# Kernel tuning notes

Hardware: AMD Instinct MI355X
Metric: run time of the kernel (lower is better)

The kernel has to match this reference:

```python
import jax, jax.numpy as jnp
import numpy as np

N, SD, HD, CD, AD = 8192, 64, 128, 32, 8  # num_agents, state_dim, hidden_dim, comm_dim, action_dim
NOISE_SCALE = 0.01


def _l2norm(x, axis):
    # F.normalize: x / max(||x||_2, eps), eps=1e-12
    return x / jnp.maximum(jnp.linalg.norm(x, axis=axis, keepdims=True), 1e-12)


def setup_inputs() -> dict:
    key = jax.random.key(0)
    ks = jax.random.split(key, 12)
    def w(k, shape, scale=0.05):
        return jax.random.normal(k, shape, jnp.float32) * scale
    return {
        "states": jax.random.normal(ks[0], (N, SD), jnp.float32),
        "noise": jax.random.normal(ks[1], (N, HD), jnp.float32),
        # ReasoningCore: Linear(SD+CD->HD), ReLU, Linear(HD->HD)
        "W1": w(ks[2], (SD + CD, HD)), "b1": jnp.zeros((HD,), jnp.float32),
        "W2": w(ks[3], (HD, HD)),      "b2": jnp.zeros((HD,), jnp.float32),
        # CommunicationModule encoder: Linear(HD->CD)
        "Wc": w(ks[4], (HD, CD)), "bc": jnp.zeros((CD,), jnp.float32),
        # GNNLayer: Linear(HD->HD)
        "Wg": w(ks[5], (HD, HD)), "bg": jnp.zeros((HD,), jnp.float32),
        # Policy: Linear(HD->AD)
        "Wp": w(ks[6], (HD, AD)), "bp": jnp.zeros((AD,), jnp.float32),
        # Value: Linear(HD->1)
        "Wv": w(ks[7], (HD, 1)), "bv": jnp.zeros((1,), jnp.float32),
        # RoleHead: Linear(HD->3)
        "Wr": w(ks[8], (HD, 3)), "br": jnp.zeros((3,), jnp.float32),
    }


def reference(states, noise, W1, b1, W2, b2, Wc, bc, Wg, bg, Wp, bp, Wv, bv, Wr, br):
    def core(x, comm):
        h = jax.nn.relu(jnp.concatenate([x, comm], axis=-1) @ W1 + b1)  # [N, HD]
        return h @ W2 + b2

    comm0 = jnp.zeros((N, CD), states.dtype)
    H = core(states, comm0)                                   # [N, HD]
    msgs = _l2norm(H @ Wc + bc, axis=1)                       # [N, CD]
    comm = jnp.broadcast_to(msgs.mean(axis=0, keepdims=True), (N, CD))
    H = core(states, comm)                                    # [N, HD]
    adj = jnp.ones((N, N), states.dtype) / N                  # dense uniform adjacency
    H = jax.nn.relu((adj @ H) @ Wg + bg)                      # GNN layer
    H = _l2norm(H + noise * NOISE_SCALE, axis=1)
    actions = jnp.tanh(H @ Wp + bp)                           # [N, AD]
    values = H @ Wv + bv                                      # [N, 1]
    role_probs = jax.nn.softmax(H @ Wr + br, axis=-1)         # [N, 3]
    return (H, actions, values, role_probs)
```

## Files before the change

kernel.cpp:

```cpp
#include <hip/hip_runtime.h>
#include <math.h>

#define N_AG 8192
#define SD 64
#define HD 128
#define CD 32
#define AD 8

#define P_OFF     0
#define W2C_OFF   (N_AG*HD)
#define BCP_OFF   (W2C_OFF + HD*CD)
#define MSUM_OFF  (BCP_OFF + CD)
#define HSUM_OFF  (MSUM_OFF + CD)
#define G_OFF     (HSUM_OFF + HD)

__global__ void k0_pre(const float* __restrict__ W2, const float* __restrict__ b2,
                       const float* __restrict__ Wc, const float* __restrict__ bc,
                       float* __restrict__ ws) {
    float* W2c  = ws + W2C_OFF;
    float* bcp  = ws + BCP_OFF;
    float* msum = ws + MSUM_OFF;
    float* hsum = ws + HSUM_OFF;
    int tid = threadIdx.x;
    if (blockIdx.x < 16) {
        int idx = blockIdx.x * 256 + tid;
        int i = idx >> 5, c = idx & 31;
        float s = 0.f;
        #pragma unroll 8
        for (int k = 0; k < HD; ++k) s += W2[i*HD + k] * Wc[k*CD + c];
        W2c[idx] = s;
    } else {
        if (tid < CD) {
            float s = bc[tid];
            for (int k = 0; k < HD; ++k) s += b2[k] * Wc[k*CD + tid];
            bcp[tid] = s;
            msum[tid] = 0.f;
        }
        if (tid >= 64 && tid < 64 + HD) hsum[tid - 64] = 0.f;
    }
}

#define APB1 16
__global__ void k1_phaseA(const float* __restrict__ X, const float* __restrict__ W1,
                          const float* __restrict__ b1, float* __restrict__ ws) {
    const float* W2c = ws + W2C_OFF;
    const float* bcp = ws + BCP_OFF;
    float* P    = ws + P_OFF;
    float* msum = ws + MSUM_OFF;
    __shared__ float sX[APB1][SD];
    __shared__ float sH[APB1][HD + 1];
    __shared__ float sM[APB1][CD + 1];
    __shared__ float sR[APB1];
    int tid = threadIdx.x;
    int a0 = blockIdx.x * APB1;
    for (int i = tid; i < APB1 * SD; i += 256) sX[i >> 6][i & 63] = X[a0 * SD + i];
    __syncthreads();
    for (int idx = tid; idx < APB1 * HD; idx += 256) {
        int ag = idx >> 7, c = idx & 127;
        float s = b1[c];
        #pragma unroll
        for (int k = 0; k < SD; ++k) s += sX[ag][k] * W1[k*HD + c];
        P[(a0 + ag)*HD + c] = s;
        sH[ag][c] = fmaxf(s, 0.f);
    }
    __syncthreads();
    for (int idx = tid; idx < APB1 * CD; idx += 256) {
        int ag = idx >> 5, c = idx & 31;
        float s = bcp[c];
        #pragma unroll 16
        for (int k = 0; k < HD; ++k) s += sH[ag][k] * W2c[k*CD + c];
        sM[ag][c] = s;
    }
    __syncthreads();
    if (tid < APB1) {
        float ss = 0.f;
        for (int c = 0; c < CD; ++c) { float m = sM[tid][c]; ss += m * m; }
        sR[tid] = 1.f / fmaxf(sqrtf(ss), 1e-12f);
    }
    __syncthreads();
    if (tid < CD) {
        float s = 0.f;
        for (int ag = 0; ag < APB1; ++ag) s += sM[ag][tid] * sR[ag];
        atomicAdd(&msum[tid], s);
    }
}

#define APB2 16
__global__ void k2_phaseB(const float* __restrict__ W1, float* __restrict__ ws) {
    const float* P    = ws + P_OFF;
    const float* msum = ws + MSUM_OFF;
    float* hsum = ws + HSUM_OFF;
    __shared__ float cvec[HD];
    __shared__ float red[256];
    int tid = threadIdx.x;
    if (tid < HD) {
        float s = 0.f;
        #pragma unroll
        for (int k = 0; k < CD; ++k) s += msum[k] * W1[(SD + k)*HD + tid];
        cvec[tid] = s * (1.f / (float)N_AG);
    }
    __syncthreads();
    int c = tid & 127, half = tid >> 7;
    int a0 = blockIdx.x * APB2;
    float part = 0.f;
    for (int ag = half; ag < APB2; ag += 2)
        part += fmaxf(P[(a0 + ag)*HD + c] + cvec[c], 0.f);
    red[tid] = part;
    __syncthreads();
    if (tid < HD) atomicAdd(&hsum[tid], red[tid] + red[tid + 128]);
}

__global__ void k3_gvec(const float* __restrict__ W2, const float* __restrict__ b2,
                        const float* __restrict__ Wg, const float* __restrict__ bg,
                        float* __restrict__ ws) {
    const float* hsum = ws + HSUM_OFF;
    float* g = ws + G_OFF;
    __shared__ float hm[HD];
    __shared__ float u[HD];
    int t = threadIdx.x;
    hm[t] = hsum[t] * (1.f / (float)N_AG);
    __syncthreads();
    float s = b2[t];
    #pragma unroll 16
    for (int k = 0; k < HD; ++k) s += hm[k] * W2[k*HD + t];
    u[t] = s;
    __syncthreads();
    float s2 = bg[t];
    #pragma unroll 16
    for (int k = 0; k < HD; ++k) s2 += u[k] * Wg[k*HD + t];
    g[t] = fmaxf(s2, 0.f);
}

__global__ void k4_out(const float* __restrict__ noise,
                       const float* __restrict__ Wp, const float* __restrict__ bp,
                       const float* __restrict__ Wv, const float* __restrict__ bv,
                       const float* __restrict__ Wr, const float* __restrict__ br,
                       const float* __restrict__ ws, float* __restrict__ out) {
    const float* g = ws + G_OFF;
    int gtid = blockIdx.x * blockDim.x + threadIdx.x;
    int a = gtid >> 6;
    int lane = threadIdx.x & 63;
    if (a >= N_AG) return;
    float v0 = g[lane]      + 0.01f * noise[a*HD + lane];
    float v1 = g[lane + 64] + 0.01f * noise[a*HD + 64 + lane];
    float ss = v0 * v0 + v1 * v1;
    #pragma unroll
    for (int off = 32; off; off >>= 1) ss += __shfl_xor(ss, off);
    float rinv = 1.f / fmaxf(sqrtf(ss), 1e-12f);
    float h0 = v0 * rinv, h1 = v1 * rinv;
    float* outH = out;
    float* outA = out + N_AG * HD;
    float* outV = outA + N_AG * AD;
    float* outR = outV + N_AG;
    outH[a*HD + lane]      = h0;
    outH[a*HD + 64 + lane] = h1;
    float acc[12];
    #pragma unroll
    for (int j = 0; j < 8; ++j)
        acc[j] = h0 * Wp[lane*AD + j] + h1 * Wp[(lane + 64)*AD + j];
    acc[8] = h0 * Wv[lane] + h1 * Wv[lane + 64];
    #pragma unroll
    for (int j = 0; j < 3; ++j)
        acc[9 + j] = h0 * Wr[lane*3 + j] + h1 * Wr[(lane + 64)*3 + j];
    #pragma unroll
    for (int j = 0; j < 12; ++j) {
        #pragma unroll
        for (int off = 32; off; off >>= 1) acc[j] += __shfl_xor(acc[j], off);
    }
    if (lane < 8) {
        outA[a*AD + lane] = tanhf(acc[lane] + bp[lane]);
    } else if (lane == 8) {
        outV[a] = acc[8] + bv[0];
    } else if (lane >= 9 && lane < 12) {
        float l0 = acc[9] + br[0], l1 = acc[10] + br[1], l2 = acc[11] + br[2];
        float m = fmaxf(l0, fmaxf(l1, l2));
        float e0 = expf(l0 - m), e1 = expf(l1 - m), e2 = expf(l2 - m);
        float denom = e0 + e1 + e2;
        float mine = (lane == 9) ? e0 : (lane == 10) ? e1 : e2;
        outR[a*3 + (lane - 9)] = mine / denom;
    }
}

extern "C" void kernel_launch(void* const* d_in, const int* in_sizes, int n_in,
                              void* d_out, int out_size, void* d_ws, size_t ws_size,
                              hipStream_t stream) {
    const float* states = (const float*)d_in[0];
    const float* noise  = (const float*)d_in[1];
    const float* W1 = (const float*)d_in[2];
    const float* b1 = (const float*)d_in[3];
    const float* W2 = (const float*)d_in[4];
    const float* b2 = (const float*)d_in[5];
    const float* Wc = (const float*)d_in[6];
    const float* bc = (const float*)d_in[7];
    const float* Wg = (const float*)d_in[8];
    const float* bg = (const float*)d_in[9];
    const float* Wp = (const float*)d_in[10];
    const float* bp = (const float*)d_in[11];
    const float* Wv = (const float*)d_in[12];
    const float* bv = (const float*)d_in[13];
    const float* Wr = (const float*)d_in[14];
    const float* br = (const float*)d_in[15];
    float* ws  = (float*)d_ws;
    float* out = (float*)d_out;

    hipLaunchKernelGGL(k0_pre,   dim3(17),           dim3(256), 0, stream, W2, b2, Wc, bc, ws);
    hipLaunchKernelGGL(k1_phaseA,dim3(N_AG / APB1),  dim3(256), 0, stream, states, W1, b1, ws);
    hipLaunchKernelGGL(k2_phaseB,dim3(N_AG / APB2),  dim3(256), 0, stream, W1, ws);
    hipLaunchKernelGGL(k3_gvec,  dim3(1),            dim3(128), 0, stream, W2, b2, Wg, bg, ws);
    hipLaunchKernelGGL(k4_out,   dim3(N_AG / 4),     dim3(256), 0, stream, noise, Wp, bp, Wv, bv, Wr, br, ws, out);
}
```

Before: 142.1 us.

## Vectorize phase kernels, fuse gvec into output kernel, transpose head weights

Rewrites the pipeline. k3 (the single-block g-vector kernel) is folded into the output kernel, and every block recomputes the 128-wide g vector redundantly. The per-agent kernels now use float4 register tiling with two agents per thread. The policy, value and role weights are pre-transposed into a packed workspace array so the heads become per-lane dot products instead of 12 full-wavefront shuffle reductions. This removes one launch and many shuffles, but each of the 512 output blocks now repeats two 128x128 matvecs.

```diff
diff --git a/kernel.cpp b/kernel.cpp
--- a/kernel.cpp
+++ b/kernel.cpp
@@ -8,176 +8,231 @@
 #define AD 8
 
 #define P_OFF     0
-#define W2C_OFF   (N_AG*HD)
-#define BCP_OFF   (W2C_OFF + HD*CD)
+#define W2CT_OFF  (N_AG*HD)
+#define WALLT_OFF (W2CT_OFF + CD*HD)
+#define BALL_OFF  (WALLT_OFF + 12*HD)
+#define BCP_OFF   (BALL_OFF + 16)
 #define MSUM_OFF  (BCP_OFF + CD)
 #define HSUM_OFF  (MSUM_OFF + CD)
-#define G_OFF     (HSUM_OFF + HD)
 
 __global__ void k0_pre(const float* __restrict__ W2, const float* __restrict__ b2,
                        const float* __restrict__ Wc, const float* __restrict__ bc,
-                       float* __restrict__ ws) {
-    float* W2c  = ws + W2C_OFF;
-    float* bcp  = ws + BCP_OFF;
-    float* msum = ws + MSUM_OFF;
-    float* hsum = ws + HSUM_OFF;
-    int tid = threadIdx.x;
-    if (blockIdx.x < 16) {
-        int idx = blockIdx.x * 256 + tid;
-        int i = idx >> 5, c = idx & 31;
-        float s = 0.f;
-        #pragma unroll 8
-        for (int k = 0; k < HD; ++k) s += W2[i*HD + k] * Wc[k*CD + c];
-        W2c[idx] = s;
-    } else {
-        if (tid < CD) {
-            float s = bc[tid];
-            for (int k = 0; k < HD; ++k) s += b2[k] * Wc[k*CD + tid];
-            bcp[tid] = s;
-            msum[tid] = 0.f;
-        }
-        if (tid >= 64 && tid < 64 + HD) hsum[tid - 64] = 0.f;
-    }
-}
-
-#define APB1 16
-__global__ void k1_phaseA(const float* __restrict__ X, const float* __restrict__ W1,
-                          const float* __restrict__ b1, float* __restrict__ ws) {
-    const float* W2c = ws + W2C_OFF;
-    const float* bcp = ws + BCP_OFF;
-    float* P    = ws + P_OFF;
-    float* msum = ws + MSUM_OFF;
-    __shared__ float sX[APB1][SD];
-    __shared__ float sH[APB1][HD + 1];
-    __shared__ float sM[APB1][CD + 1];
-    __shared__ float sR[APB1];
-    int tid = threadIdx.x;
-    int a0 = blockIdx.x * APB1;
-    for (int i = tid; i < APB1 * SD; i += 256) sX[i >> 6][i & 63] = X[a0 * SD + i];
-    __syncthreads();
-    for (int idx = tid; idx < APB1 * HD; idx += 256) {
-        int ag = idx >> 7, c = idx & 127;
-        float s = b1[c];
-        #pragma unroll
-        for (int k = 0; k < SD; ++k) s += sX[ag][k] * W1[k*HD + c];
-        P[(a0 + ag)*HD + c] = s;
-        sH[ag][c] = fmaxf(s, 0.f);
-    }
-    __syncthreads();
-    for (int idx = tid; idx < APB1 * CD; idx += 256) {
-        int ag = idx >> 5, c = idx & 31;
-        float s = bcp[c];
-        #pragma unroll 16
-        for (int k = 0; k < HD; ++k) s += sH[ag][k] * W2c[k*CD + c];
-        sM[ag][c] = s;
-    }
-    __syncthreads();
-    if (tid < APB1) {
-        float ss = 0.f;
-        for (int c = 0; c < CD; ++c) { float m = sM[tid][c]; ss += m * m; }
-        sR[tid] = 1.f / fmaxf(sqrtf(ss), 1e-12f);
-    }
-    __syncthreads();
-    if (tid < CD) {
-        float s = 0.f;
-        for (int ag = 0; ag < APB1; ++ag) s += sM[ag][tid] * sR[ag];
-        atomicAdd(&msum[tid], s);
-    }
-}
-
-#define APB2 16
-__global__ void k2_phaseB(const float* __restrict__ W1, float* __restrict__ ws) {
-    const float* P    = ws + P_OFF;
-    const float* msum = ws + MSUM_OFF;
-    float* hsum = ws + HSUM_OFF;
-    __shared__ float cvec[HD];
-    __shared__ float red[256];
-    int tid = threadIdx.x;
-    if (tid < HD) {
-        float s = 0.f;
-        #pragma unroll
-        for (int k = 0; k < CD; ++k) s += msum[k] * W1[(SD + k)*HD + tid];
-        cvec[tid] = s * (1.f / (float)N_AG);
-    }
-    __syncthreads();
-    int c = tid & 127, half = tid >> 7;
-    int a0 = blockIdx.x * APB2;
-    float part = 0.f;
-    for (int ag = half; ag < APB2; ag += 2)
-        part += fmaxf(P[(a0 + ag)*HD + c] + cvec[c], 0.f);
-    red[tid] = part;
-    __syncthreads();
-    if (tid < HD) atomicAdd(&hsum[tid], red[tid] + red[tid + 128]);
-}
-
-__global__ void k3_gvec(const float* __restrict__ W2, const float* __restrict__ b2,
-                        const float* __restrict__ Wg, const float* __restrict__ bg,
-                        float* __restrict__ ws) {
-    const float* hsum = ws + HSUM_OFF;
-    float* g = ws + G_OFF;
-    __shared__ float hm[HD];
-    __shared__ float u[HD];
-    int t = threadIdx.x;
-    hm[t] = hsum[t] * (1.f / (float)N_AG);
-    __syncthreads();
-    float s = b2[t];
-    #pragma unroll 16
-    for (int k = 0; k < HD; ++k) s += hm[k] * W2[k*HD + t];
-    u[t] = s;
-    __syncthreads();
-    float s2 = bg[t];
-    #pragma unroll 16
-    for (int k = 0; k < HD; ++k) s2 += u[k] * Wg[k*HD + t];
-    g[t] = fmaxf(s2, 0.f);
-}
-
-__global__ void k4_out(const float* __restrict__ noise,
                        const float* __restrict__ Wp, const float* __restrict__ bp,
                        const float* __restrict__ Wv, const float* __restrict__ bv,
                        const float* __restrict__ Wr, const float* __restrict__ br,
-                       const float* __restrict__ ws, float* __restrict__ out) {
-    const float* g = ws + G_OFF;
-    int gtid = blockIdx.x * blockDim.x + threadIdx.x;
-    int a = gtid >> 6;
-    int lane = threadIdx.x & 63;
-    if (a >= N_AG) return;
-    float v0 = g[lane]      + 0.01f * noise[a*HD + lane];
-    float v1 = g[lane + 64] + 0.01f * noise[a*HD + 64 + lane];
-    float ss = v0 * v0 + v1 * v1;
-    #pragma unroll
-    for (int off = 32; off; off >>= 1) ss += __shfl_xor(ss, off);
+                       float* __restrict__ ws) {
+    int t = threadIdx.x, b = blockIdx.x;
+    if (b < 16) {
+        int idx = b * 256 + t;
+        int c = idx & 31, k = idx >> 5;
+        float s = 0.f;
+        #pragma unroll 16
+        for (int j = 0; j < HD; ++j) s += W2[k*HD + j] * Wc[j*CD + c];
+        ws[W2CT_OFF + c*HD + k] = s;
+    } else if (b == 16) {
+        if (t < CD) {
+            float s = bc[t];
+            for (int j = 0; j < HD; ++j) s += b2[j] * Wc[j*CD + t];
+            ws[BCP_OFF + t] = s;
+            ws[MSUM_OFF + t] = 0.f;
+        } else if (t >= 64 && t < 192) {
+            ws[HSUM_OFF + t - 64] = 0.f;
+        }
+    } else {
+        for (int idx = t; idx < 12 * HD; idx += 256) {
+            int j = idx >> 7, k = idx & 127;
+            float v = (j < 8) ? Wp[k*AD + j] : (j == 8) ? Wv[k] : Wr[k*3 + (j - 9)];
+            ws[WALLT_OFF + idx] = v;
+        }
+        if (t < 12) ws[BALL_OFF + t] = (t < 8) ? bp[t] : (t == 8) ? bv[0] : br[t - 9];
+    }
+}
+
+#define FMA4(acc, xv, w0, w1, w2, w3)                                   \
+    acc.x += xv.x*w0.x + xv.y*w1.x + xv.z*w2.x + xv.w*w3.x;             \
+    acc.y += xv.x*w0.y + xv.y*w1.y + xv.z*w2.y + xv.w*w3.y;             \
+    acc.z += xv.x*w0.z + xv.y*w1.z + xv.z*w2.z + xv.w*w3.z;             \
+    acc.w += xv.x*w0.w + xv.y*w1.w + xv.z*w2.w + xv.w*w3.w;
+
+__global__ __launch_bounds__(256) void k1(const float* __restrict__ X,
+                                          const float* __restrict__ W1,
+                                          const float* __restrict__ b1,
+                                          float* __restrict__ ws) {
+    __shared__ float4 sX4[16][16];
+    __shared__ float4 sT4[16][32];
+    __shared__ float  sMg[16][32];
+    int t = threadIdx.x;
+    int a0 = blockIdx.x * 16;
+    {
+        int ag = t >> 4, k4 = t & 15;
+        sX4[ag][k4] = ((const float4*)X)[(a0 + ag)*16 + k4];
+    }
+    __syncthreads();
+    const int c4 = t & 31;
+    const int A0 = t >> 5, A1 = A0 + 8;
+    float4 bb = ((const float4*)b1)[c4];
+    float4 acc0 = bb, acc1 = bb;
+    #pragma unroll
+    for (int k4 = 0; k4 < 16; ++k4) {
+        float4 xA = sX4[A0][k4], xB = sX4[A1][k4];
+        float4 w0 = ((const float4*)(W1 + (4*k4 + 0)*HD))[c4];
+        float4 w1 = ((const float4*)(W1 + (4*k4 + 1)*HD))[c4];
+        float4 w2 = ((const float4*)(W1 + (4*k4 + 2)*HD))[c4];
+        float4 w3 = ((const float4*)(W1 + (4*k4 + 3)*HD))[c4];
+        FMA4(acc0, xA, w0, w1, w2, w3);
+        FMA4(acc1, xB, w0, w1, w2, w3);
+    }
+    ((float4*)(ws + P_OFF))[(a0 + A0)*32 + c4] = acc0;
+    ((float4*)(ws + P_OFF))[(a0 + A1)*32 + c4] = acc1;
+    float4 r0, r1;
+    r0.x = fmaxf(acc0.x, 0.f); r0.y = fmaxf(acc0.y, 0.f); r0.z = fmaxf(acc0.z, 0.f); r0.w = fmaxf(acc0.w, 0.f);
+    r1.x = fmaxf(acc1.x, 0.f); r1.y = fmaxf(acc1.y, 0.f); r1.z = fmaxf(acc1.z, 0.f); r1.w = fmaxf(acc1.w, 0.f);
+    sT4[A0][c4] = r0;
+    sT4[A1][c4] = r1;
+    __syncthreads();
+    float m0 = ws[BCP_OFF + c4], m1 = m0;
+    const float4* w2cT = (const float4*)(ws + W2CT_OFF);
+    #pragma unroll
+    for (int k4 = 0; k4 < 32; ++k4) {
+        float4 ta = sT4[A0][k4], tb = sT4[A1][k4];
+        float4 wc = w2cT[c4*32 + k4];
+        m0 += ta.x*wc.x + ta.y*wc.y + ta.z*wc.z + ta.w*wc.w;
+        m1 += tb.x*wc.x + tb.y*wc.y + tb.z*wc.z + tb.w*wc.w;
+    }
+    float ss0 = m0*m0, ss1 = m1*m1;
+    #pragma unroll
+    for (int off = 1; off < 32; off <<= 1) {
+        ss0 += __shfl_xor(ss0, off);
+        ss1 += __shfl_xor(ss1, off);
+    }
+    float rv0 = 1.f / fmaxf(sqrtf(ss0), 1e-12f);
+    float rv1 = 1.f / fmaxf(sqrtf(ss1), 1e-12f);
+    sMg[A0][c4] = m0 * rv0;
+    sMg[A1][c4] = m1 * rv1;
+    __syncthreads();
+    if (t < 32) {
+        float s = 0.f;
+        #pragma unroll
+        for (int ag = 0; ag < 16; ++ag) s += sMg[ag][t];
+        atomicAdd(&ws[MSUM_OFF + t], s);
+    }
+}
+
+__global__ __launch_bounds__(256) void k2(const float* __restrict__ W1,
+                                          float* __restrict__ ws) {
+    __shared__ __align__(16) float sC[HD];
+    __shared__ float4 sRed[8][32];
+    int t = threadIdx.x;
+    int a0 = blockIdx.x * 32;
+    if (t < HD) {
+        float s = 0.f;
+        #pragma unroll
+        for (int k = 0; k < CD; ++k) s += ws[MSUM_OFF + k] * W1[(SD + k)*HD + t];
+        sC[t] = s * (1.f / (float)N_AG);
+    }
+    __syncthreads();
+    const int c4 = t & 31, g = t >> 5;
+    float4 cv = ((const float4*)sC)[c4];
+    float4 acc; acc.x = acc.y = acc.z = acc.w = 0.f;
+    #pragma unroll
+    for (int i = 0; i < 4; ++i) {
+        int ag = g + i*8;
+        float4 p = ((const float4*)(ws + P_OFF))[(a0 + ag)*32 + c4];
+        acc.x += fmaxf(p.x + cv.x, 0.f);
+        acc.y += fmaxf(p.y + cv.y, 0.f);
+        acc.z += fmaxf(p.z + cv.z, 0.f);
+        acc.w += fmaxf(p.w + cv.w, 0.f);
+    }
+    sRed[g][c4] = acc;
+    __syncthreads();
+    if (t < 32) {
+        float4 s = sRed[0][t];
+        #pragma unroll
+        for (int gg = 1; gg < 8; ++gg) {
+            float4 v = sRed[gg][t];
+            s.x += v.x; s.y += v.y; s.z += v.z; s.w += v.w;
+        }
+        atomicAdd(&ws[HSUM_OFF + 4*t + 0], s.x);
+        atomicAdd(&ws[HSUM_OFF + 4*t + 1], s.y);
+        atomicAdd(&ws[HSUM_OFF + 4*t + 2], s.z);
+        atomicAdd(&ws[HSUM_OFF + 4*t + 3], s.w);
+    }
+}
+
+__global__ __launch_bounds__(256) void k34(const float* __restrict__ noise,
+                                           const float* __restrict__ W2, const float* __restrict__ b2,
+                                           const float* __restrict__ Wg, const float* __restrict__ bg,
+                                           float* __restrict__ ws, float* __restrict__ out) {
+    __shared__ __align__(16) float sA[HD];
+    __shared__ __align__(16) float sB[HD];
+    __shared__ __align__(16) float sG[HD];
+    __shared__ float4 sH4[16][32];
+    int t = threadIdx.x;
+    int a0 = blockIdx.x * 16;
+    if (t < HD) sA[t] = ws[HSUM_OFF + t] * (1.f / (float)N_AG);
+    __syncthreads();
+    if (t < HD) {
+        float s = b2[t];
+        #pragma unroll 16
+        for (int k = 0; k < HD; ++k) s += sA[k] * W2[k*HD + t];
+        sB[t] = s;
+    }
+    __syncthreads();
+    if (t < HD) {
+        float s = bg[t];
+        #pragma unroll 16
+        for (int k = 0; k < HD; ++k) s += sB[k] * Wg[k*HD + t];
+        sG[t] = fmaxf(s, 0.f);
+    }
+    __syncthreads();
+    const int ag = t >> 4, q = t & 15;
+    const int a = a0 + ag;
+    float4 n0 = ((const float4*)noise)[a*32 + q*2];
+    float4 n1 = ((const float4*)noise)[a*32 + q*2 + 1];
+    float4 g0 = ((const float4*)sG)[q*2];
+    float4 g1 = ((const float4*)sG)[q*2 + 1];
+    float4 v0, v1;
+    v0.x = g0.x + 0.01f*n0.x; v0.y = g0.y + 0.01f*n0.y; v0.z = g0.z + 0.01f*n0.z; v0.w = g0.w + 0.01f*n0.w;
+    v1.x = g1.x + 0.01f*n1.x; v1.y = g1.y + 0.01f*n1.y; v1.z = g1.z + 0.01f*n1.z; v1.w = g1.w + 0.01f*n1.w;
+    float ss = v0.x*v0.x + v0.y*v0.y + v0.z*v0.z + v0.w*v0.w
+             + v1.x*v1.x + v1.y*v1.y + v1.z*v1.z + v1.w*v1.w;
+    #pragma unroll
+    for (int off = 1; off < 16; off <<= 1) ss += __shfl_xor(ss, off);
     float rinv = 1.f / fmaxf(sqrtf(ss), 1e-12f);
-    float h0 = v0 * rinv, h1 = v1 * rinv;
-    float* outH = out;
-    float* outA = out + N_AG * HD;
-    float* outV = outA + N_AG * AD;
+    float4 h0, h1;
+    h0.x = v0.x*rinv; h0.y = v0.y*rinv; h0.z = v0.z*rinv; h0.w = v0.w*rinv;
+    h1.x = v1.x*rinv; h1.y = v1.y*rinv; h1.z = v1.z*rinv; h1.w = v1.w*rinv;
+    ((float4*)out)[a*32 + q*2]     = h0;
+    ((float4*)out)[a*32 + q*2 + 1] = h1;
+    sH4[ag][q*2]     = h0;
+    sH4[ag][q*2 + 1] = h1;
+    __syncthreads();
+    float acc = 0.f;
+    if (q < 12) {
+        acc = ws[BALL_OFF + q];
+        const float4* wT = (const float4*)(ws + WALLT_OFF);
+        #pragma unroll
+        for (int k4 = 0; k4 < 32; ++k4) {
+            float4 hh = sH4[ag][k4];
+            float4 w  = wT[q*32 + k4];
+            acc += hh.x*w.x + hh.y*w.y + hh.z*w.z + hh.w*w.w;
+        }
+    }
+    int base = (t & 63) & ~15;
+    float a9  = __shfl(acc, base + 9, 64);
+    float a10 = __shfl(acc, base + 10, 64);
+    float a11 = __shfl(acc, base + 11, 64);
+    float* outA = out + N_AG*HD;
+    float* outV = outA + N_AG*AD;
     float* outR = outV + N_AG;
-    outH[a*HD + lane]      = h0;
-    outH[a*HD + 64 + lane] = h1;
-    float acc[12];
-    #pragma unroll
-    for (int j = 0; j < 8; ++j)
-        acc[j] = h0 * Wp[lane*AD + j] + h1 * Wp[(lane + 64)*AD + j];
-    acc[8] = h0 * Wv[lane] + h1 * Wv[lane + 64];
-    #pragma unroll
-    for (int j = 0; j < 3; ++j)
-        acc[9 + j] = h0 * Wr[lane*3 + j] + h1 * Wr[(lane + 64)*3 + j];
-    #pragma unroll
-    for (int j = 0; j < 12; ++j) {
-        #pragma unroll
-        for (int off = 32; off; off >>= 1) acc[j] += __shfl_xor(acc[j], off);
-    }
-    if (lane < 8) {
-        outA[a*AD + lane] = tanhf(acc[lane] + bp[lane]);
-    } else if (lane == 8) {
-        outV[a] = acc[8] + bv[0];
-    } else if (lane >= 9 && lane < 12) {
-        float l0 = acc[9] + br[0], l1 = acc[10] + br[1], l2 = acc[11] + br[2];
-        float m = fmaxf(l0, fmaxf(l1, l2));
-        float e0 = expf(l0 - m), e1 = expf(l1 - m), e2 = expf(l2 - m);
-        float denom = e0 + e1 + e2;
-        float mine = (lane == 9) ? e0 : (lane == 10) ? e1 : e2;
-        outR[a*3 + (lane - 9)] = mine / denom;
+    if (q < 8) {
+        outA[a*AD + q] = tanhf(acc);
+    } else if (q == 8) {
+        outV[a] = acc;
+    } else if (q < 12) {
+        float m = fmaxf(a9, fmaxf(a10, a11));
+        float d = expf(a9 - m) + expf(a10 - m) + expf(a11 - m);
+        outR[a*3 + (q - 9)] = expf(acc - m) / d;
     }
 }
 
@@ -203,9 +258,10 @@
     float* ws  = (float*)d_ws;
     float* out = (float*)d_out;
 
-    hipLaunchKernelGGL(k0_pre,   dim3(17),           dim3(256), 0, stream, W2, b2, Wc, bc, ws);
-    hipLaunchKernelGGL(k1_phaseA,dim3(N_AG / APB1),  dim3(256), 0, stream, states, W1, b1, ws);
-    hipLaunchKernelGGL(k2_phaseB,dim3(N_AG / APB2),  dim3(256), 0, stream, W1, ws);
-    hipLaunchKernelGGL(k3_gvec,  dim3(1),            dim3(128), 0, stream, W2, b2, Wg, bg, ws);
-    hipLaunchKernelGGL(k4_out,   dim3(N_AG / 4),     dim3(256), 0, stream, noise, Wp, bp, Wv, bv, Wr, br, ws, out);
-}
+    hipLaunchKernelGGL(k0_pre, dim3(18),  dim3(256), 0, stream,
+                       W2, b2, Wc, bc, Wp, bp, Wv, bv, Wr, br, ws);
+    hipLaunchKernelGGL(k1,     dim3(512), dim3(256), 0, stream, states, W1, b1, ws);
+    hipLaunchKernelGGL(k2,     dim3(256), dim3(256), 0, stream, W1, ws);
+    hipLaunchKernelGGL(k34,    dim3(512), dim3(256), 0, stream,
+                       noise, W2, b2, Wg, bg, ws, out);
+}
```

Measured after the change: 149.0 us. +4.9%, slower.
